# Performance work log

Hardware: AMD Instinct MI355X
Metric: run time of the kernel (lower is better)

Reference implementation:

```python
import jax, jax.numpy as jnp
import numpy as np

B, T, C = 2, 4096, 768
H = 12
HD = C // H  # 64

def setup_inputs() -> dict:
    key = jax.random.key(0)
    k1, k2, k3 = jax.random.split(key, 3)
    scale_in = 1.0 / np.sqrt(C)
    return {
        "x": jax.random.normal(k1, (B, T, C), dtype=jnp.float32),
        "w_qkv": jax.random.normal(k2, (C, 3 * C), dtype=jnp.float32) * scale_in,
        "b_qkv": jnp.zeros((3 * C,), dtype=jnp.float32),
        "w_proj": jax.random.normal(k3, (C, C), dtype=jnp.float32) * scale_in,
        "b_proj": jnp.zeros((C,), dtype=jnp.float32),
    }

def reference(x, w_qkv, b_qkv, w_proj, b_proj):
    # Dropout in eval mode (identity), matching module.eval().
    Bx, Tx, Cx = x.shape
    qkv = x @ w_qkv + b_qkv                      # [B,T,3C]
    q, k, v = jnp.split(qkv, 3, axis=-1)
    def to_heads(t):
        return t.reshape(Bx, Tx, H, HD).transpose(0, 2, 1, 3)  # [B,H,T,hd]
    q, k, v = to_heads(q), to_heads(k), to_heads(v)
    att = jnp.einsum('bhqd,bhkd->bhqk', q, k) / jnp.sqrt(jnp.float32(HD))
    causal = jnp.tril(jnp.ones((Tx, Tx), dtype=bool))
    att = jnp.where(causal[None, None], att, -jnp.inf)
    att = jax.nn.softmax(att, axis=-1)
    y = jnp.einsum('bhqk,bhkd->bhqd', att, v)    # [B,H,T,hd]
    y = y.transpose(0, 2, 1, 3).reshape(Bx, Tx, Cx)
    return y @ w_proj + b_proj
```

## Files before the change

kernel.cpp:

```cpp
#include <hip/hip_runtime.h>


#define TSEQ 4096
#define NH 12
#define CDIM 768

typedef __bf16 bf16;
typedef __attribute__((ext_vector_type(8))) __bf16 bf16x8;
typedef __attribute__((ext_vector_type(4))) __bf16 bf16x4;
typedef __attribute__((ext_vector_type(4))) float f32x4;

__device__ __forceinline__ void gload16(const void* g, void* l) {
  __builtin_amdgcn_global_load_lds(
      (const __attribute__((address_space(1))) void*)g,
      (__attribute__((address_space(3))) void*)l, 16, 0, 0);
}

__device__ __forceinline__ float fexp2(float x) {
  return __builtin_amdgcn_exp2f(x);
}

#define MAX3(a, b, c) fmaxf(fmaxf((a), (b)), (c))

__global__ void convert_x_kernel(const float* __restrict__ x,
                                 bf16* __restrict__ xb, int n) {
  int i = (blockIdx.x * blockDim.x + threadIdx.x) * 4;
  if (i < n) {
    float4 v = *(const float4*)(x + i);
    bf16x4 o;
    o[0] = (bf16)v.x; o[1] = (bf16)v.y; o[2] = (bf16)v.z; o[3] = (bf16)v.w;
    *(bf16x4*)(xb + i) = o;
  }
}

__global__ void transpose_w_kernel(const float* __restrict__ src,
                                   bf16* __restrict__ dst, int R, int Cc) {
  __shared__ float tile[32][33];
  int tx = threadIdx.x, ty = threadIdx.y;
  int c0 = blockIdx.x * 32, r0 = blockIdx.y * 32;
#pragma unroll
  for (int i = 0; i < 4; ++i)
    tile[ty + i * 8][tx] = src[(size_t)(r0 + ty + i * 8) * Cc + c0 + tx];
  __syncthreads();
#pragma unroll
  for (int i = 0; i < 4; ++i)
    dst[(size_t)(c0 + ty + i * 8) * R + r0 + tx] = (bf16)tile[tx][ty + i * 8];
}

template <int MODE>
__global__ __launch_bounds__(256) void gemm_kernel(
    const bf16* __restrict__ A, const bf16* __restrict__ BT,
    const float* __restrict__ bias, bf16* __restrict__ qk_out,
    bf16* __restrict__ vT_out, float* __restrict__ c_out) {
  constexpr int K = 768;
  __shared__ alignas(16) bf16 As[128 * 64];
  __shared__ alignas(16) bf16 Bs[128 * 64];
  const int t = threadIdx.x;
  const int l = t & 63, w = t >> 6;
  const int l15 = l & 15, lg = l >> 4;
  const int nwg = gridDim.x * gridDim.y;
  int id = blockIdx.y * gridDim.x + blockIdx.x;
  id = (id & 7) * (nwg >> 3) + (id >> 3);
  const int m0 = (id / gridDim.x) << 7, n0 = (id % gridDim.x) << 7;
  const int wr = w >> 1, wc = w & 1;

  f32x4 acc[4][4] = {};

  const int r0 = t >> 3;
  const int kb8 = (((t & 7) ^ (r0 & 7)) << 3);
  const bf16* Asrc = A + (size_t)(m0 + r0) * K + kb8;
  const bf16* Bsrc = BT + (size_t)(n0 + r0) * K + kb8;

  for (int kt = 0; kt < K / 64; ++kt) {
#pragma unroll
    for (int i = 0; i < 4; ++i)
      gload16(Asrc + kt * 64 + (size_t)i * 32 * K, (char*)As + w * 1024 + i * 4096);
#pragma unroll
    for (int i = 0; i < 4; ++i)
      gload16(Bsrc + kt * 64 + (size_t)i * 32 * K, (char*)Bs + w * 1024 + i * 4096);
    __syncthreads();
#pragma unroll
    for (int kk = 0; kk < 2; ++kk) {
      bf16x8 af[4], bfv[4];
#pragma unroll
      for (int m = 0; m < 4; ++m) {
        int r = (wr << 6) + (m << 4) + l15;
        int kb = (kk << 2) + lg;
        af[m] = *(const bf16x8*)((const char*)As + r * 128 + ((kb ^ (r & 7)) << 4));
      }
#pragma unroll
      for (int n = 0; n < 4; ++n) {
        int r = (wc << 6) + (n << 4) + l15;
        int kb = (kk << 2) + lg;
        bfv[n] = *(const bf16x8*)((const char*)Bs + r * 128 + ((kb ^ (r & 7)) << 4));
      }
#pragma unroll
      for (int m = 0; m < 4; ++m)
#pragma unroll
        for (int n = 0; n < 4; ++n)
          acc[m][n] = __builtin_amdgcn_mfma_f32_16x16x32_bf16(af[m], bfv[n],
                                                              acc[m][n], 0, 0, 0);
    }
    __syncthreads();
  }

#pragma unroll
  for (int m = 0; m < 4; ++m) {
    int row = m0 + (wr << 6) + (m << 4) + (lg << 2);
    int b = row >> 12, tt = row & 4095;
#pragma unroll
    for (int n = 0; n < 4; ++n) {
      int col = n0 + (wc << 6) + (n << 4) + l15;
      float bv = bias[col];
      if (MODE == 0) {
        if (col < 1536) {
          float sc = (col < 768) ? 0.18033688011112042f : 1.0f;
          bf16* dst = qk_out + (size_t)(b * TSEQ + tt) * 1536 + col;
#pragma unroll
          for (int j = 0; j < 4; ++j)
            dst[(size_t)j * 1536] = (bf16)((acc[m][n][j] + bv) * sc);
        } else {
          int nl = col - 1536;
          bf16* dst = vT_out +
              ((size_t)(b * NH + (nl >> 6)) * 64 + (nl & 63)) * TSEQ + tt;
#pragma unroll
          for (int j = 0; j < 4; ++j) dst[j] = (bf16)(acc[m][n][j] + bv);
        }
      } else {
        float* dst = c_out + (size_t)row * 768 + col;
#pragma unroll
        for (int j = 0; j < 4; ++j) dst[(size_t)j * 768] = acc[m][n][j] + bv;
      }
    }
  }
}

__global__ __launch_bounds__(256) void attn_kernel(
    const bf16* __restrict__ qk,
    const bf16* __restrict__ vT,
    bf16* __restrict__ y) {
  __shared__ alignas(16) char lds[40960];
  const int t = threadIdx.x;
  const int l = t & 63, w = t >> 6;
  const int l15 = l & 15, lg = l >> 4;
  const int nwg = gridDim.x * gridDim.y;
  int id = blockIdx.y * gridDim.x + blockIdx.x;
  id = (id & 7) * (nwg >> 3) + (id >> 3);
  const int qb = 63 - (id & 63);
  const int bh = id >> 6;
  const int b = bh / NH, h = bh % NH;
  const bf16* qbase = qk + (size_t)b * TSEQ * 1536 + h * 64;
  const bf16* kbase = qbase + 768;
  const bf16* vbase = vT + (size_t)bh * 64 * TSEQ;

  const int r0 = t >> 3;
  const int kb8 = (((t & 7) ^ (r0 & 7)) << 3);
  const int q0 = qb << 6;
  const int nkt = qb + 1;
  const int qw = q0 + (w << 4);

  const int swz = l15 & 7;
  int koff[2];
  koff[0] = l15 * 128 + ((lg ^ swz) << 4);
  koff[1] = l15 * 128 + (((4 + lg) ^ swz) << 4);
  char* const preg = lds + w * 2048;
  const char* par[2] = {preg + koff[0], preg + koff[1]};
  char* pwa[4];
#pragma unroll
  for (int m = 0; m < 4; ++m)
    pwa[m] = preg + l15 * 128 + ((((m << 5) + (lg << 3)) ^ (swz << 4)));
  char* const stA = lds + w * 1024;
  const bf16* ksrc = kbase + (size_t)(64 + r0) * 1536 + kb8;
  const bf16* vsrc = vbase + (size_t)r0 * TSEQ + 64 + kb8;

#pragma unroll
  for (int i = 0; i < 2; ++i) {
    gload16(qbase + (size_t)(q0 + i * 32 + r0) * 1536 + kb8, stA + i * 4096);
    gload16(kbase + (size_t)(i * 32 + r0) * 1536 + kb8,
            lds + 0x2000 + w * 1024 + i * 4096);
    gload16(vbase + (size_t)(i * 32 + r0) * TSEQ + kb8,
            lds + 0x4000 + w * 1024 + i * 4096);
  }
  __syncthreads();

  bf16x8 qf[2];
#pragma unroll
  for (int kk = 0; kk < 2; ++kk) {
    int r = (w << 4) + l15;
    int kb = (kk << 2) + lg;
    qf[kk] = *(const bf16x8*)(lds + r * 128 + ((kb ^ (r & 7)) << 4));
  }

  f32x4 o[4] = {};
  float mrun = -__builtin_inff();
  float lrun = 0.f;
  int kreg = 0x2000;

  for (int kt = 0; kt < nkt; ++kt) {
    const int kv0 = kt << 6;

    if (kt + 1 < nkt) {
      const int nreg = kreg ^ 0x4000;
#pragma unroll
      for (int i = 0; i < 2; ++i) {
        gload16(ksrc + (size_t)i * 32 * 1536, lds + nreg + w * 1024 + i * 4096);
        gload16(vsrc + (size_t)i * 32 * TSEQ,
                lds + nreg + 0x2000 + w * 1024 + i * 4096);
      }
      ksrc += (size_t)64 * 1536;
      vsrc += 64;
    }

    f32x4 s[4] = {};
    __builtin_amdgcn_s_setprio(1);
#pragma unroll
    for (int kk = 0; kk < 2; ++kk) {
#pragma unroll
      for (int m = 0; m < 4; ++m) {
        bf16x8 kf = *(const bf16x8*)(lds + kreg + koff[kk] + m * 2048);
        s[m] = __builtin_amdgcn_mfma_f32_16x16x32_bf16(kf, qf[kk], s[m], 0, 0, 0);
      }
    }
    __builtin_amdgcn_s_setprio(0);

    if (kv0 + 63 > qw) {
      int q = qw + l15;
#pragma unroll
      for (int m = 0; m < 4; ++m) {
        int kvr = kv0 + (m << 4) + (lg << 2);
#pragma unroll
        for (int j = 0; j < 4; ++j)
          if (kvr + j > q) s[m][j] = -__builtin_inff();
      }
    }
    float t0 = MAX3(s[0][0], s[0][1], s[0][2]);
    float t1 = MAX3(s[0][3], s[1][0], s[1][1]);
    float t2 = MAX3(s[1][2], s[1][3], s[2][0]);
    float t3 = MAX3(s[2][1], s[2][2], s[2][3]);
    float t4 = MAX3(s[3][0], s[3][1], s[3][2]);
    float cmax = MAX3(MAX3(t0, t1, s[3][3]), fmaxf(t2, t3), t4);
    cmax = fmaxf(cmax, __shfl_xor(cmax, 16));
    cmax = fmaxf(cmax, __shfl_xor(cmax, 32));
    if (__any(cmax > mrun + 8.f)) {
      float mnew = fmaxf(mrun, cmax);
      float alpha = fexp2(mrun - mnew);
      mrun = mnew;
      lrun *= alpha;
#pragma unroll
      for (int j = 0; j < 4; ++j) {
        int rr = (lg << 2) + j;
        float a = __shfl(alpha, (l & 48) | rr);
#pragma unroll
        for (int no = 0; no < 4; ++no) o[no][j] *= a;
      }
    }
    float ps = 0.f;
#pragma unroll
    for (int m = 0; m < 4; ++m)
#pragma unroll
      for (int j = 0; j < 4; ++j) {
        float pv = fexp2(s[m][j] - mrun);
        s[m][j] = pv;
        ps += pv;
      }
    ps += __shfl_xor(ps, 16);
    ps += __shfl_xor(ps, 32);
    lrun += ps;
#pragma unroll
    for (int m = 0; m < 4; ++m) {
      bf16x4 pv;
#pragma unroll
      for (int j = 0; j < 4; ++j) pv[j] = (bf16)s[m][j];
      *(bf16x4*)(pwa[m]) = pv;
    }
    __builtin_amdgcn_s_setprio(1);
#pragma unroll
    for (int kk = 0; kk < 2; ++kk) {
      bf16x8 pa = *(const bf16x8*)(par[kk]);
#pragma unroll
      for (int no = 0; no < 4; ++no) {
        bf16x8 vb = *(const bf16x8*)(lds + kreg + 0x2000 + koff[kk] + no * 2048);
        o[no] = __builtin_amdgcn_mfma_f32_16x16x32_bf16(pa, vb, o[no], 0, 0, 0);
      }
    }
    __builtin_amdgcn_s_setprio(0);
    __syncthreads();
    kreg ^= 0x4000;
  }

#pragma unroll
  for (int j = 0; j < 4; ++j) {
    int rr = (lg << 2) + j;
    float lv = __shfl(lrun, (l & 48) | rr);
    float linv = 1.0f / lv;
    int qrow = qw + rr;
    size_t base = ((size_t)(b * TSEQ + qrow)) * 768 + h * 64;
#pragma unroll
    for (int no = 0; no < 4; ++no)
      y[base + (no << 4) + l15] = (bf16)(o[no][j] * linv);
  }
}

extern "C" void kernel_launch(void* const* d_in, const int* in_sizes, int n_in,
                              void* d_out, int out_size, void* d_ws,
                              size_t ws_size, hipStream_t stream) {
  const float* x = (const float*)d_in[0];
  const float* w_qkv = (const float*)d_in[1];
  const float* b_qkv = (const float*)d_in[2];
  const float* w_proj = (const float*)d_in[3];
  const float* b_proj = (const float*)d_in[4];
  float* out = (float*)d_out;
  char* ws = (char*)d_ws;

  bf16* xb     = (bf16*)(ws);
  bf16* wqkvT  = (bf16*)(ws + 12582912);
  bf16* wprojT = (bf16*)(ws + 16121856);
  bf16* qkbuf  = (bf16*)(ws + 17301504);
  bf16* vTbuf  = (bf16*)(ws + 42467328);
  bf16* ybuf   = (bf16*)(ws + 55050240);

  convert_x_kernel<<<6144, 256, 0, stream>>>(x, xb, 2 * TSEQ * CDIM);
  transpose_w_kernel<<<dim3(72, 24), dim3(32, 8), 0, stream>>>(w_qkv, wqkvT, 768, 2304);
  transpose_w_kernel<<<dim3(24, 24), dim3(32, 8), 0, stream>>>(w_proj, wprojT, 768, 768);
  gemm_kernel<0><<<dim3(18, 64), 256, 0, stream>>>(xb, wqkvT, b_qkv, qkbuf, vTbuf, nullptr);
  attn_kernel<<<dim3(64, 24), 256, 0, stream>>>(qkbuf, vTbuf, ybuf);
  gemm_kernel<1><<<dim3(6, 64), 256, 0, stream>>>(ybuf, wprojT, b_proj, nullptr, nullptr, out);
}
```

Baseline: 250.9 us.

## Split long causal attention rows across two workgroups and add combine kernel

```diff
diff --git a/kernel.cpp b/kernel.cpp
--- a/kernel.cpp
+++ b/kernel.cpp
@@ -138,16 +138,29 @@
 __global__ __launch_bounds__(256) void attn_kernel(
     const bf16* __restrict__ qk,
     const bf16* __restrict__ vT,
-    bf16* __restrict__ y) {
-  __shared__ alignas(16) char lds[40960];
+    bf16* __restrict__ y,
+    bf16* __restrict__ opart,
+    float* __restrict__ mlb) {
+  __shared__ alignas(16) char lds[24576];
   const int t = threadIdx.x;
   const int l = t & 63, w = t >> 6;
   const int l15 = l & 15, lg = l >> 4;
-  const int nwg = gridDim.x * gridDim.y;
-  int id = blockIdx.y * gridDim.x + blockIdx.x;
-  id = (id & 7) * (nwg >> 3) + (id >> 3);
-  const int qb = 63 - (id & 63);
-  const int bh = id >> 6;
+
+  const int rk = blockIdx.x;
+  const int xcd = rk & 7, s = rk >> 3;
+  const int bh = xcd * 3 + (s % 3);
+  const int j = s / 3;
+  int qb, kt0, kt1, half, split;
+  if (j < 64) {
+    int i = j >> 1;
+    qb = 63 - i; half = j & 1; split = 1;
+    int nk = qb + 1, nh0 = (nk + 1) >> 1;
+    kt0 = half ? nh0 : 0;
+    kt1 = half ? nk : nh0;
+  } else {
+    qb = 95 - j; half = 0; split = 0;
+    kt0 = 0; kt1 = qb + 1;
+  }
   const int b = bh / NH, h = bh % NH;
   const bf16* qbase = qk + (size_t)b * TSEQ * 1536 + h * 64;
   const bf16* kbase = qbase + 768;
@@ -156,7 +169,6 @@
   const int r0 = t >> 3;
   const int kb8 = (((t & 7) ^ (r0 & 7)) << 3);
   const int q0 = qb << 6;
-  const int nkt = qb + 1;
   const int qw = q0 + (w << 4);
 
   const int swz = l15 & 7;
@@ -169,17 +181,26 @@
 #pragma unroll
   for (int m = 0; m < 4; ++m)
     pwa[m] = preg + l15 * 128 + ((((m << 5) + (lg << 3)) ^ (swz << 4)));
-  char* const stA = lds + w * 1024;
-  const bf16* ksrc = kbase + (size_t)(64 + r0) * 1536 + kb8;
-  const bf16* vsrc = vbase + (size_t)r0 * TSEQ + 64 + kb8;
 
 #pragma unroll
   for (int i = 0; i < 2; ++i) {
-    gload16(qbase + (size_t)(q0 + i * 32 + r0) * 1536 + kb8, stA + i * 4096);
-    gload16(kbase + (size_t)(i * 32 + r0) * 1536 + kb8,
+    gload16(qbase + (size_t)(q0 + i * 32 + r0) * 1536 + kb8,
+            lds + w * 1024 + i * 4096);
+    gload16(kbase + (size_t)(kt0 * 64 + i * 32 + r0) * 1536 + kb8,
             lds + 0x2000 + w * 1024 + i * 4096);
-    gload16(vbase + (size_t)(i * 32 + r0) * TSEQ + kb8,
+    gload16(vbase + (size_t)(i * 32 + r0) * TSEQ + kt0 * 64 + kb8,
             lds + 0x4000 + w * 1024 + i * 4096);
+  }
+  const bf16* ksrc = kbase + (size_t)((kt0 + 1) * 64 + r0) * 1536 + kb8;
+  const bf16* vsrc = vbase + (size_t)r0 * TSEQ + (kt0 + 1) * 64 + kb8;
+  int4 kr0, kr1, vr0, vr1;
+  if (kt0 + 1 < kt1) {
+    kr0 = *(const int4*)(ksrc);
+    kr1 = *(const int4*)(ksrc + (size_t)32 * 1536);
+    vr0 = *(const int4*)(vsrc);
+    vr1 = *(const int4*)(vsrc + (size_t)32 * TSEQ);
+    ksrc += (size_t)64 * 1536;
+    vsrc += 64;
   }
   __syncthreads();
 
@@ -194,31 +215,18 @@
   f32x4 o[4] = {};
   float mrun = -__builtin_inff();
   float lrun = 0.f;
-  int kreg = 0x2000;
-
-  for (int kt = 0; kt < nkt; ++kt) {
+
+  for (int kt = kt0; kt < kt1; ++kt) {
     const int kv0 = kt << 6;
 
-    if (kt + 1 < nkt) {
-      const int nreg = kreg ^ 0x4000;
-#pragma unroll
-      for (int i = 0; i < 2; ++i) {
-        gload16(ksrc + (size_t)i * 32 * 1536, lds + nreg + w * 1024 + i * 4096);
-        gload16(vsrc + (size_t)i * 32 * TSEQ,
-                lds + nreg + 0x2000 + w * 1024 + i * 4096);
-      }
-      ksrc += (size_t)64 * 1536;
-      vsrc += 64;
-    }
-
-    f32x4 s[4] = {};
+    f32x4 s4[4] = {};
     __builtin_amdgcn_s_setprio(1);
 #pragma unroll
     for (int kk = 0; kk < 2; ++kk) {
 #pragma unroll
       for (int m = 0; m < 4; ++m) {
-        bf16x8 kf = *(const bf16x8*)(lds + kreg + koff[kk] + m * 2048);
-        s[m] = __builtin_amdgcn_mfma_f32_16x16x32_bf16(kf, qf[kk], s[m], 0, 0, 0);
+        bf16x8 kf = *(const bf16x8*)(lds + 0x2000 + koff[kk] + m * 2048);
+        s4[m] = __builtin_amdgcn_mfma_f32_16x16x32_bf16(kf, qf[kk], s4[m], 0, 0, 0);
       }
     }
     __builtin_amdgcn_s_setprio(0);
@@ -229,16 +237,16 @@
       for (int m = 0; m < 4; ++m) {
         int kvr = kv0 + (m << 4) + (lg << 2);
 #pragma unroll
-        for (int j = 0; j < 4; ++j)
-          if (kvr + j > q) s[m][j] = -__builtin_inff();
-      }
-    }
-    float t0 = MAX3(s[0][0], s[0][1], s[0][2]);
-    float t1 = MAX3(s[0][3], s[1][0], s[1][1]);
-    float t2 = MAX3(s[1][2], s[1][3], s[2][0]);
-    float t3 = MAX3(s[2][1], s[2][2], s[2][3]);
-    float t4 = MAX3(s[3][0], s[3][1], s[3][2]);
-    float cmax = MAX3(MAX3(t0, t1, s[3][3]), fmaxf(t2, t3), t4);
+        for (int jj = 0; jj < 4; ++jj)
+          if (kvr + jj > q) s4[m][jj] = -__builtin_inff();
+      }
+    }
+    float t0 = MAX3(s4[0][0], s4[0][1], s4[0][2]);
+    float t1 = MAX3(s4[0][3], s4[1][0], s4[1][1]);
+    float t2 = MAX3(s4[1][2], s4[1][3], s4[2][0]);
+    float t3 = MAX3(s4[2][1], s4[2][2], s4[2][3]);
+    float t4 = MAX3(s4[3][0], s4[3][1], s4[3][2]);
+    float cmax = MAX3(MAX3(t0, t1, s4[3][3]), fmaxf(t2, t3), t4);
     cmax = fmaxf(cmax, __shfl_xor(cmax, 16));
     cmax = fmaxf(cmax, __shfl_xor(cmax, 32));
     if (__any(cmax > mrun + 8.f)) {
@@ -247,20 +255,20 @@
       mrun = mnew;
       lrun *= alpha;
 #pragma unroll
-      for (int j = 0; j < 4; ++j) {
-        int rr = (lg << 2) + j;
+      for (int jj = 0; jj < 4; ++jj) {
+        int rr = (lg << 2) + jj;
         float a = __shfl(alpha, (l & 48) | rr);
 #pragma unroll
-        for (int no = 0; no < 4; ++no) o[no][j] *= a;
+        for (int no = 0; no < 4; ++no) o[no][jj] *= a;
       }
     }
     float ps = 0.f;
 #pragma unroll
     for (int m = 0; m < 4; ++m)
 #pragma unroll
-      for (int j = 0; j < 4; ++j) {
-        float pv = fexp2(s[m][j] - mrun);
-        s[m][j] = pv;
+      for (int jj = 0; jj < 4; ++jj) {
+        float pv = fexp2(s4[m][jj] - mrun);
+        s4[m][jj] = pv;
         ps += pv;
       }
     ps += __shfl_xor(ps, 16);
@@ -270,7 +278,7 @@
     for (int m = 0; m < 4; ++m) {
       bf16x4 pv;
 #pragma unroll
-      for (int j = 0; j < 4; ++j) pv[j] = (bf16)s[m][j];
+      for (int jj = 0; jj < 4; ++jj) pv[jj] = (bf16)s4[m][jj];
       *(bf16x4*)(pwa[m]) = pv;
     }
     __builtin_amdgcn_s_setprio(1);
@@ -279,26 +287,90 @@
       bf16x8 pa = *(const bf16x8*)(par[kk]);
 #pragma unroll
       for (int no = 0; no < 4; ++no) {
-        bf16x8 vb = *(const bf16x8*)(lds + kreg + 0x2000 + koff[kk] + no * 2048);
+        bf16x8 vb = *(const bf16x8*)(lds + 0x4000 + koff[kk] + no * 2048);
         o[no] = __builtin_amdgcn_mfma_f32_16x16x32_bf16(pa, vb, o[no], 0, 0, 0);
       }
     }
     __builtin_amdgcn_s_setprio(0);
-    __syncthreads();
-    kreg ^= 0x4000;
-  }
-
-#pragma unroll
-  for (int j = 0; j < 4; ++j) {
-    int rr = (lg << 2) + j;
-    float lv = __shfl(lrun, (l & 48) | rr);
-    float linv = 1.0f / lv;
-    int qrow = qw + rr;
-    size_t base = ((size_t)(b * TSEQ + qrow)) * 768 + h * 64;
-#pragma unroll
-    for (int no = 0; no < 4; ++no)
-      y[base + (no << 4) + l15] = (bf16)(o[no][j] * linv);
-  }
+
+    if (kt + 1 < kt1) {
+      __syncthreads();
+      *(int4*)(lds + 0x2000 + t * 16) = kr0;
+      *(int4*)(lds + 0x2000 + 4096 + t * 16) = kr1;
+      *(int4*)(lds + 0x4000 + t * 16) = vr0;
+      *(int4*)(lds + 0x4000 + 4096 + t * 16) = vr1;
+      if (kt + 2 < kt1) {
+        kr0 = *(const int4*)(ksrc);
+        kr1 = *(const int4*)(ksrc + (size_t)32 * 1536);
+        vr0 = *(const int4*)(vsrc);
+        vr1 = *(const int4*)(vsrc + (size_t)32 * TSEQ);
+        ksrc += (size_t)64 * 1536;
+        vsrc += 64;
+      }
+      __syncthreads();
+    }
+  }
+
+  if (!split) {
+#pragma unroll
+    for (int jj = 0; jj < 4; ++jj) {
+      int rr = (lg << 2) + jj;
+      float lv = __shfl(lrun, (l & 48) | rr);
+      float linv = 1.0f / lv;
+      int qrow = qw + rr;
+      size_t base = ((size_t)(b * TSEQ + qrow)) * 768 + h * 64;
+#pragma unroll
+      for (int no = 0; no < 4; ++no)
+        y[base + (no << 4) + l15] = (bf16)(o[no][jj] * linv);
+    }
+  } else {
+    const int sb2 = (bh * 32 + (qb - 32)) * 2 + half;
+#pragma unroll
+    for (int jj = 0; jj < 4; ++jj) {
+      int rr = (lg << 2) + jj;
+      float lv = __shfl(lrun, (l & 48) | rr);
+      float linv = 1.0f / lv;
+      int r = (w << 4) + rr;
+      size_t base = ((size_t)sb2 * 64 + r) * 64;
+#pragma unroll
+      for (int no = 0; no < 4; ++no)
+        opart[base + (no << 4) + l15] = (bf16)(o[no][jj] * linv);
+    }
+    if (l < 16) {
+      size_t mi = ((size_t)sb2 * 64 + (w << 4) + l) * 2;
+      mlb[mi] = mrun;
+      mlb[mi + 1] = lrun;
+    }
+  }
+}
+
+__global__ void combine_kernel(const bf16* __restrict__ op,
+                               const float* __restrict__ ml,
+                               bf16* __restrict__ y) {
+  int g = blockIdx.x * 256 + threadIdx.x;
+  int d4 = (g & 15) << 2;
+  int rid = g >> 4;
+  int rr = rid & 63;
+  int sb = rid >> 6;
+  int bh = sb >> 5, qb = 32 + (sb & 31);
+  int b = bh / NH, h = bh % NH;
+  size_t m0i = ((size_t)(sb * 2) * 64 + rr) * 2;
+  size_t m1i = ((size_t)(sb * 2 + 1) * 64 + rr) * 2;
+  float m0 = ml[m0i], l0 = ml[m0i + 1];
+  float m1 = ml[m1i], l1 = ml[m1i + 1];
+  float M = fmaxf(m0, m1);
+  float w0 = fexp2(m0 - M) * l0, w1 = fexp2(m1 - M) * l1;
+  float inv = 1.f / (w0 + w1);
+  w0 *= inv; w1 *= inv;
+  const bf16* o0 = op + (((size_t)(sb * 2) * 64 + rr) * 64 + d4);
+  const bf16* o1 = op + (((size_t)(sb * 2 + 1) * 64 + rr) * 64 + d4);
+  bf16x4 a = *(const bf16x4*)o0, c = *(const bf16x4*)o1;
+  bf16x4 out;
+#pragma unroll
+  for (int jj = 0; jj < 4; ++jj)
+    out[jj] = (bf16)(w0 * (float)a[jj] + w1 * (float)c[jj]);
+  int qrow = (qb << 6) + rr;
+  *(bf16x4*)(y + ((size_t)(b * TSEQ + qrow)) * 768 + h * 64 + d4) = out;
 }
 
 extern "C" void kernel_launch(void* const* d_in, const int* in_sizes, int n_in,
@@ -318,11 +390,13 @@
   bf16* qkbuf  = (bf16*)(ws + 17301504);
   bf16* vTbuf  = (bf16*)(ws + 42467328);
   bf16* ybuf   = (bf16*)(ws + 55050240);
+  float* mlb   = (float*)(ws + 67633152);
 
   convert_x_kernel<<<6144, 256, 0, stream>>>(x, xb, 2 * TSEQ * CDIM);
   transpose_w_kernel<<<dim3(72, 24), dim3(32, 8), 0, stream>>>(w_qkv, wqkvT, 768, 2304);
   transpose_w_kernel<<<dim3(24, 24), dim3(32, 8), 0, stream>>>(w_proj, wprojT, 768, 768);
   gemm_kernel<0><<<dim3(18, 64), 256, 0, stream>>>(xb, wqkvT, b_qkv, qkbuf, vTbuf, nullptr);
-  attn_kernel<<<dim3(64, 24), 256, 0, stream>>>(qkbuf, vTbuf, ybuf);
+  attn_kernel<<<2304, 256, 0, stream>>>(qkbuf, vTbuf, ybuf, xb, mlb);
+  combine_kernel<<<3072, 256, 0, stream>>>(xb, mlb, ybuf);
   gemm_kernel<1><<<dim3(6, 64), 256, 0, stream>>>(ybuf, wprojT, b_proj, nullptr, nullptr, out);
 }
```

New measurement: 247.7 us. No clear change (-1.3%).
